# Kernel optimization log

Measured on AMD Instinct MI355X. Metric: run time of the kernel, lower is better.

Reference implementation:

```python
import jax, jax.numpy as jnp
import numpy as np

IN_DIM = 2048
OUT_DIM = 2048
GRID_SIZE = 8
BATCH = 4096
LN_EPS = 1e-5


def setup_inputs() -> dict:
    key = jax.random.key(0)
    k_x, k_w = jax.random.split(key)
    x = jax.random.normal(k_x, (BATCH, IN_DIM), dtype=jnp.float32)
    spline_weight = jax.random.normal(k_w, (OUT_DIM, IN_DIM, GRID_SIZE), dtype=jnp.float32) * 0.1
    return {
        "x": x,
        "ln_weight": jnp.ones((IN_DIM,), jnp.float32),
        "ln_bias": jnp.zeros((IN_DIM,), jnp.float32),
        "spline_weight": spline_weight,
        "scale_base": jnp.ones((OUT_DIM, IN_DIM), jnp.float32),
        "bias": jnp.zeros((OUT_DIM,), jnp.float32),
        "rbf_beta": jnp.full((1,), 2.0, jnp.float32),
        "grid": jnp.linspace(-1.0, 1.0, GRID_SIZE, dtype=jnp.float32),
    }


def reference(x, ln_weight, ln_bias, spline_weight, scale_base, bias, rbf_beta, grid):
    # LayerNorm over last dim (eps=1e-5, elementwise affine)
    mu = jnp.mean(x, axis=-1, keepdims=True)
    var = jnp.mean(jnp.square(x - mu), axis=-1, keepdims=True)
    xn = (x - mu) * jax.lax.rsqrt(var + LN_EPS) * ln_weight + ln_bias  # (B, in)

    beta = jnp.clip(rbf_beta, 0.5, 6.0)  # (1,)
    # RBF basis: (B, in, G)
    basis = jnp.exp(-jnp.square(xn[..., None] - grid) * beta)

    # Torch einsum('bdig,oid->bod') broadcasts the singleton d of basis against
    # spline_weight's last axis and sums g; after .sum(-1) this equals
    # (sum_g basis) @ (sum_d spline_weight).T
    S = basis.sum(-1)              # (B, in)
    Wd = spline_weight.sum(-1)     # (out, in)
    spline_sum = jnp.einsum('bi,oi->bo', S, Wd)

    base_out = jnp.einsum('bi,oi->bo', xn, scale_base)
    return base_out + spline_sum + bias
```

## Files before the change

### kernel.cpp

```cpp
#include <hip/hip_runtime.h>
#include <hip/hip_bf16.h>
#include <stdint.h>

constexpr int IN_DIM   = 2048;
constexpr int OUT_DIM  = 2048;
constexpr int BATCH    = 4096;
constexpr int KDIM     = 2 * IN_DIM;
constexpr float LN_EPS = 1e-5f;

#define TILE 128
#define BK   64
constexpr int NK    = KDIM / BK;
constexpr int STAGE = TILE * BK;

typedef __attribute__((ext_vector_type(8))) short  short8;
typedef __attribute__((ext_vector_type(4))) float  f32x4;

__device__ __forceinline__ unsigned short f2bf(float f) {
  __hip_bfloat16 h = __float2bfloat16(f);
  return *reinterpret_cast<unsigned short*>(&h);
}
__device__ __forceinline__ unsigned pack2bf(float a, float b) {
  return (unsigned)f2bf(a) | ((unsigned)f2bf(b) << 16);
}

constexpr int SW_F4   = OUT_DIM * IN_DIM * 2;
constexpr int SB_F4   = OUT_DIM * IN_DIM / 4;
constexpr int PACK_BLOCKS = (SW_F4 + SB_F4) / 256;

__global__ __launch_bounds__(256) void prep_kernel(
    const float* __restrict__ x, const float* __restrict__ lnw,
    const float* __restrict__ lnb, const float* __restrict__ betap,
    const float* __restrict__ grid, unsigned short* __restrict__ A,
    const float* __restrict__ sw, const float* __restrict__ sb,
    unsigned* __restrict__ Bu)
{
  const int tid = threadIdx.x;
  if (blockIdx.x < BATCH) {
    const int row = blockIdx.x;
    const float4* xr = reinterpret_cast<const float4*>(x + (size_t)row * IN_DIM);
    float4 v0 = xr[tid];
    float4 v1 = xr[tid + 256];
    float s = (v0.x + v0.y) + (v0.z + v0.w) + (v1.x + v1.y) + (v1.z + v1.w);
    float q = v0.x * v0.x + v0.y * v0.y + v0.z * v0.z + v0.w * v0.w
            + v1.x * v1.x + v1.y * v1.y + v1.z * v1.z + v1.w * v1.w;
    #pragma unroll
    for (int off = 32; off > 0; off >>= 1) {
      s += __shfl_down(s, off, 64);
      q += __shfl_down(q, off, 64);
    }
    __shared__ float red[10];
    const int lane = tid & 63, wv = tid >> 6;
    if (lane == 0) { red[wv] = s; red[4 + wv] = q; }
    __syncthreads();
    if (tid == 0) {
      float ts = (red[0] + red[1]) + (red[2] + red[3]);
      float tq = (red[4] + red[5]) + (red[6] + red[7]);
      float mu  = ts * (1.0f / IN_DIM);
      float var = tq * (1.0f / IN_DIM) - mu * mu;
      red[8] = mu;
      red[9] = rsqrtf(var + LN_EPS);
    }
    __syncthreads();
    const float mu = red[8], rs = red[9];
    const float beta = fminf(fmaxf(betap[0], 0.5f), 6.0f);
    float g[8];
    #pragma unroll
    for (int i = 0; i < 8; i++) g[i] = grid[i];
    const float4* w4 = reinterpret_cast<const float4*>(lnw);
    const float4* b4 = reinterpret_cast<const float4*>(lnb);
    unsigned short* Ar = A + (size_t)row * KDIM;
    #pragma unroll
    for (int h = 0; h < 2; h++) {
      const int idx = tid + h * 256;
      float4 xv  = (h == 0) ? v0 : v1;
      float4 wv4 = w4[idx];
      float4 bv4 = b4[idx];
      float xa[4] = {xv.x, xv.y, xv.z, xv.w};
      float wa[4] = {wv4.x, wv4.y, wv4.z, wv4.w};
      float ba[4] = {bv4.x, bv4.y, bv4.z, bv4.w};
      float xn[4], S[4];
      #pragma unroll
      for (int c = 0; c < 4; c++) {
        float xnv = (xa[c] - mu) * rs * wa[c] + ba[c];
        xn[c] = xnv;
        float acc = 0.f;
        #pragma unroll
        for (int gg = 0; gg < 8; gg++) {
          float d = xnv - g[gg];
          acc += __expf(-beta * d * d);
        }
        S[c] = acc;
      }
      uint2 px, ps;
      px.x = pack2bf(xn[0], xn[1]);
      px.y = pack2bf(xn[2], xn[3]);
      ps.x = pack2bf(S[0], S[1]);
      ps.y = pack2bf(S[2], S[3]);
      *reinterpret_cast<uint2*>(Ar + idx * 4) = px;
      *reinterpret_cast<uint2*>(Ar + IN_DIM + idx * 4) = ps;
    }
  } else {
    const int g = (blockIdx.x - BATCH) * 256 + tid;
    const int lane = tid & 63;
    if (g < SW_F4) {
      float4 v = reinterpret_cast<const float4*>(sw)[g];
      float s = (v.x + v.y) + (v.z + v.w);
      s += __shfl_xor(s, 1, 64);
      float hi = __shfl_down(s, 2, 64);
      if ((lane & 3) == 0) {
        const int i_lin = g >> 1;
        const int o = i_lin >> 11;
        const int i = i_lin & (IN_DIM - 1);
        Bu[(size_t)o * (KDIM / 2) + (IN_DIM / 2) + (i >> 1)] = pack2bf(s, hi);
      }
    } else {
      const int t = g - SW_F4;
      float4 v = reinterpret_cast<const float4*>(sb)[t];
      const int o  = t >> 9;
      const int i4 = t & 511;
      uint2 u;
      u.x = pack2bf(v.x, v.y);
      u.y = pack2bf(v.z, v.w);
      *reinterpret_cast<uint2*>(&Bu[(size_t)o * (KDIM / 2) + i4 * 2]) = u;
    }
  }
}

__device__ __forceinline__ void gld_lds16(const unsigned short* g, unsigned short* l) {
  __builtin_amdgcn_global_load_lds(
      (const __attribute__((address_space(1))) void*)g,
      (__attribute__((address_space(3))) void*)l, 16, 0, 0);
}

__global__ __launch_bounds__(256) void gemm_kernel(
    const unsigned short* __restrict__ A, const unsigned short* __restrict__ Bm,
    const float* __restrict__ bias, float* __restrict__ out)
{
  __shared__ __align__(16) unsigned short As[2 * STAGE];
  __shared__ __align__(16) unsigned short Bs[2 * STAGE];
  const int tid  = threadIdx.x;
  const int lane = tid & 63;
  const int wv   = tid >> 6;
  const int wr   = wv >> 1;
  const int wc   = wv & 1;
  const int gid = blockIdx.x;
  const int sq  = gid & 7;
  const int q   = gid >> 3;
  const int m0  = ((sq >> 1) * 8 + (q >> 3)) * TILE;
  const int n0  = ((sq & 1) * 8 + (q & 7)) * TILE;
  const int lrow = lane & 15;
  const int lkq  = lane >> 4;

  f32x4 acc[4][4] = {};

  const unsigned short* Ap[4];
  const unsigned short* Bp[4];
  unsigned short* ldsA[4];
  unsigned short* ldsB[4];
  #pragma unroll
  for (int j = 0; j < 4; j++) {
    const int seg  = j * 256 + wv * 64 + lane;
    const int row  = seg >> 3;
    const int gcol = ((seg & 7) ^ (row & 7)) * 8;
    Ap[j] = A  + (size_t)(m0 + row) * KDIM + gcol;
    Bp[j] = Bm + (size_t)(n0 + row) * KDIM + gcol;
    ldsA[j] = &As[(j * 256 + wv * 64) * 8];
    ldsB[j] = &Bs[(j * 256 + wv * 64) * 8];
  }

  #pragma unroll
  for (int j = 0; j < 4; j++) gld_lds16(Ap[j], ldsA[j]);
  #pragma unroll
  for (int j = 0; j < 4; j++) gld_lds16(Bp[j], ldsB[j]);

  #pragma unroll 1
  for (int kt = 0; kt < NK; kt++) {
    __syncthreads();
    const int cur = (kt & 1) * STAGE;
    if (kt + 1 < NK) {
      const int nxt = ((kt + 1) & 1) * STAGE;
      const int koff = (kt + 1) * BK;
      #pragma unroll
      for (int j = 0; j < 4; j++) gld_lds16(Ap[j] + koff, ldsA[j] + nxt);
      #pragma unroll
      for (int j = 0; j < 4; j++) gld_lds16(Bp[j] + koff, ldsB[j] + nxt);
    }

    short8 af[2][4], bf[2][4];
    #pragma unroll
    for (int h = 0; h < 2; h++) {
      #pragma unroll
      for (int mi = 0; mi < 4; mi++) {
        const int r = wr * 64 + mi * 16 + lrow;
        af[h][mi] = *reinterpret_cast<const short8*>(
            &As[cur + r * BK + (((h << 2) | lkq) ^ (lrow & 7)) * 8]);
      }
      #pragma unroll
      for (int ni = 0; ni < 4; ni++) {
        const int r = wc * 64 + ni * 16 + lrow;
        bf[h][ni] = *reinterpret_cast<const short8*>(
            &Bs[cur + r * BK + (((h << 2) | lkq) ^ (lrow & 7)) * 8]);
      }
    }
    #pragma unroll
    for (int h = 0; h < 2; h++)
      #pragma unroll
      for (int mi = 0; mi < 4; mi++)
        #pragma unroll
        for (int ni = 0; ni < 4; ni++)
          acc[mi][ni] = __builtin_amdgcn_mfma_f32_16x16x32_bf16(
              af[h][mi], bf[h][ni], acc[mi][ni], 0, 0, 0);
  }

  const int rb = (lane >> 4) * 4;
  #pragma unroll
  for (int ni = 0; ni < 4; ni++) {
    const int col = n0 + wc * 64 + ni * 16 + lrow;
    const float bv = bias[col];
    #pragma unroll
    for (int mi = 0; mi < 4; mi++) {
      const int rowm = m0 + wr * 64 + mi * 16 + rb;
      #pragma unroll
      for (int r = 0; r < 4; r++)
        out[(size_t)(rowm + r) * OUT_DIM + col] = acc[mi][ni][r] + bv;
    }
  }
}

extern "C" void kernel_launch(void* const* d_in, const int* in_sizes, int n_in,
                              void* d_out, int out_size, void* d_ws, size_t ws_size,
                              hipStream_t stream) {
  const float* x    = (const float*)d_in[0];
  const float* lnw  = (const float*)d_in[1];
  const float* lnb  = (const float*)d_in[2];
  const float* sw   = (const float*)d_in[3];
  const float* sb   = (const float*)d_in[4];
  const float* bias = (const float*)d_in[5];
  const float* beta = (const float*)d_in[6];
  const float* grid = (const float*)d_in[7];
  float* out = (float*)d_out;

  unsigned short* A = (unsigned short*)d_ws;
  unsigned short* B = A + (size_t)BATCH * KDIM;

  hipLaunchKernelGGL(prep_kernel, dim3(BATCH + PACK_BLOCKS), dim3(256), 0, stream,
                     x, lnw, lnb, beta, grid, A, sw, sb, (unsigned*)B);
  hipLaunchKernelGGL(gemm_kernel, dim3((BATCH / TILE) * (OUT_DIM / TILE)), dim3(256), 0, stream,
                     A, B, bias, out);
}
```

Measured before the change: 304.0 us.

## Use 256x128 tiles with 512 threads and a triple-buffered split-phase pipeline

Grows the GEMM block tile to 256x128 with 8 waves and replaces the double-buffered loop with a three-stage LDS ring. Each K-step is split into two half-phases, with prefetch issued between the fragment reads, explicit waitcnt/barrier scheduling and raised priority around the MFMA bursts. The aim is to hide global-load latency and cut sync overhead per FLOP. In exchange it uses more LDS per block and relies on hand-written waitcnt counts, which could be fragile.

```diff
diff --git a/kernel.cpp b/kernel.cpp
--- a/kernel.cpp
+++ b/kernel.cpp
@@ -8,10 +8,12 @@
 constexpr int KDIM     = 2 * IN_DIM;
 constexpr float LN_EPS = 1e-5f;
 
-#define TILE 128
-#define BK   64
-constexpr int NK    = KDIM / BK;
-constexpr int STAGE = TILE * BK;
+#define BM 256
+#define BN 128
+#define BK 64
+constexpr int NK     = KDIM / BK;
+constexpr int ASTAGE = BM * BK;
+constexpr int BSTAGE = BN * BK;
 
 typedef __attribute__((ext_vector_type(8))) short  short8;
 typedef __attribute__((ext_vector_type(4))) float  f32x4;
@@ -133,84 +135,137 @@
       (__attribute__((address_space(3))) void*)l, 16, 0, 0);
 }
 
-__global__ __launch_bounds__(256) void gemm_kernel(
+__global__ __launch_bounds__(512, 2) void gemm_kernel(
     const unsigned short* __restrict__ A, const unsigned short* __restrict__ Bm,
     const float* __restrict__ bias, float* __restrict__ out)
 {
-  __shared__ __align__(16) unsigned short As[2 * STAGE];
-  __shared__ __align__(16) unsigned short Bs[2 * STAGE];
+  __shared__ __align__(16) unsigned short As[3 * ASTAGE];
+  __shared__ __align__(16) unsigned short Bs[3 * BSTAGE];
   const int tid  = threadIdx.x;
   const int lane = tid & 63;
   const int wv   = tid >> 6;
   const int wr   = wv >> 1;
   const int wc   = wv & 1;
-  const int gid = blockIdx.x;
-  const int sq  = gid & 7;
-  const int q   = gid >> 3;
-  const int m0  = ((sq >> 1) * 8 + (q >> 3)) * TILE;
-  const int n0  = ((sq & 1) * 8 + (q & 7)) * TILE;
   const int lrow = lane & 15;
   const int lkq  = lane >> 4;
 
+  const int gid = blockIdx.x;
+  const int x   = gid & 7;
+  const int q   = gid >> 3;
+  const int m0  = ((x >> 1) * 4 + (q >> 3)) * BM;
+  const int n0  = ((x & 1) * 8 + (q & 7)) * BN;
+
   f32x4 acc[4][4] = {};
 
-  const unsigned short* Ap[4];
-  const unsigned short* Bp[4];
-  unsigned short* ldsA[4];
-  unsigned short* ldsB[4];
+  const unsigned short* Ag[4];
+  const unsigned short* Bg[2];
+  int ldsAo[4], ldsBo[2];
   #pragma unroll
   for (int j = 0; j < 4; j++) {
-    const int seg  = j * 256 + wv * 64 + lane;
-    const int row  = seg >> 3;
-    const int gcol = ((seg & 7) ^ (row & 7)) * 8;
-    Ap[j] = A  + (size_t)(m0 + row) * KDIM + gcol;
-    Bp[j] = Bm + (size_t)(n0 + row) * KDIM + gcol;
-    ldsA[j] = &As[(j * 256 + wv * 64) * 8];
-    ldsB[j] = &Bs[(j * 256 + wv * 64) * 8];
-  }
-
-  #pragma unroll
-  for (int j = 0; j < 4; j++) gld_lds16(Ap[j], ldsA[j]);
-  #pragma unroll
-  for (int j = 0; j < 4; j++) gld_lds16(Bp[j], ldsB[j]);
+    const int row  = j * 64 + (tid >> 3);
+    const int colg = ((tid & 7) ^ (row & 7)) * 8;
+    Ag[j]   = A + (size_t)(m0 + row) * KDIM + colg;
+    ldsAo[j] = (j * 512 + wv * 64) * 8;
+  }
+  #pragma unroll
+  for (int j = 0; j < 2; j++) {
+    const int row  = j * 64 + (tid >> 3);
+    const int colg = ((tid & 7) ^ (row & 7)) * 8;
+    Bg[j]   = Bm + (size_t)(n0 + row) * KDIM + colg;
+    ldsBo[j] = (j * 512 + wv * 64) * 8;
+  }
+
+  #pragma unroll
+  for (int j = 0; j < 4; j++) gld_lds16(Ag[j], &As[ldsAo[j]]);
+  #pragma unroll
+  for (int j = 0; j < 2; j++) gld_lds16(Bg[j], &Bs[ldsBo[j]]);
+  #pragma unroll
+  for (int j = 0; j < 4; j++) gld_lds16(Ag[j] + BK, &As[ASTAGE + ldsAo[j]]);
+  #pragma unroll
+  for (int j = 0; j < 2; j++) gld_lds16(Bg[j] + BK, &Bs[BSTAGE + ldsBo[j]]);
+  asm volatile("s_waitcnt vmcnt(6)" ::: "memory");
+  __builtin_amdgcn_s_barrier();
+
+  int rb_cur = 0;
+  int rb_pf  = 2;
 
   #pragma unroll 1
-  for (int kt = 0; kt < NK; kt++) {
-    __syncthreads();
-    const int cur = (kt & 1) * STAGE;
-    if (kt + 1 < NK) {
-      const int nxt = ((kt + 1) & 1) * STAGE;
-      const int koff = (kt + 1) * BK;
+  for (int t = 0; t < NK; ++t) {
+    const unsigned short* ar = &As[rb_cur * ASTAGE];
+    const unsigned short* br = &Bs[rb_cur * BSTAGE];
+    unsigned short*       aw = &As[rb_pf  * ASTAGE];
+    unsigned short*       bw = &Bs[rb_pf  * BSTAGE];
+    const int  koff = (t + 2) * BK;
+    const bool pf   = (t + 2 < NK);
+
+    short8 af[4], bf[4];
+
+    #pragma unroll
+    for (int mi = 0; mi < 4; mi++) {
+      const int r = wr * 64 + mi * 16 + lrow;
+      af[mi] = *reinterpret_cast<const short8*>(
+          &ar[r * BK + ((lkq ^ (lrow & 7)) * 8)]);
+    }
+    #pragma unroll
+    for (int ni = 0; ni < 4; ni++) {
+      const int r = wc * 64 + ni * 16 + lrow;
+      bf[ni] = *reinterpret_cast<const short8*>(
+          &br[r * BK + ((lkq ^ (lrow & 7)) * 8)]);
+    }
+    if (pf) {
+      gld_lds16(Ag[0] + koff, &aw[ldsAo[0]]);
+      gld_lds16(Ag[1] + koff, &aw[ldsAo[1]]);
+      gld_lds16(Bg[0] + koff, &bw[ldsBo[0]]);
+    }
+    __builtin_amdgcn_s_barrier();
+    asm volatile("s_waitcnt lgkmcnt(0)" ::: "memory");
+    __builtin_amdgcn_s_setprio(1);
+    #pragma unroll
+    for (int mi = 0; mi < 4; mi++)
       #pragma unroll
-      for (int j = 0; j < 4; j++) gld_lds16(Ap[j] + koff, ldsA[j] + nxt);
+      for (int ni = 0; ni < 4; ni++)
+        acc[mi][ni] = __builtin_amdgcn_mfma_f32_16x16x32_bf16(
+            af[mi], bf[ni], acc[mi][ni], 0, 0, 0);
+    __builtin_amdgcn_s_setprio(0);
+    __builtin_amdgcn_s_barrier();
+
+    #pragma unroll
+    for (int mi = 0; mi < 4; mi++) {
+      const int r = wr * 64 + mi * 16 + lrow;
+      af[mi] = *reinterpret_cast<const short8*>(
+          &ar[r * BK + (((4 | lkq) ^ (lrow & 7)) * 8)]);
+    }
+    #pragma unroll
+    for (int ni = 0; ni < 4; ni++) {
+      const int r = wc * 64 + ni * 16 + lrow;
+      bf[ni] = *reinterpret_cast<const short8*>(
+          &br[r * BK + (((4 | lkq) ^ (lrow & 7)) * 8)]);
+    }
+    if (pf) {
+      gld_lds16(Ag[2] + koff, &aw[ldsAo[2]]);
+      gld_lds16(Ag[3] + koff, &aw[ldsAo[3]]);
+      gld_lds16(Bg[1] + koff, &bw[ldsBo[1]]);
+    }
+    __builtin_amdgcn_s_barrier();
+    asm volatile("s_waitcnt lgkmcnt(0)" ::: "memory");
+    __builtin_amdgcn_s_setprio(1);
+    #pragma unroll
+    for (int mi = 0; mi < 4; mi++)
       #pragma unroll
-      for (int j = 0; j < 4; j++) gld_lds16(Bp[j] + koff, ldsB[j] + nxt);
-    }
-
-    short8 af[2][4], bf[2][4];
-    #pragma unroll
-    for (int h = 0; h < 2; h++) {
-      #pragma unroll
-      for (int mi = 0; mi < 4; mi++) {
-        const int r = wr * 64 + mi * 16 + lrow;
-        af[h][mi] = *reinterpret_cast<const short8*>(
-            &As[cur + r * BK + (((h << 2) | lkq) ^ (lrow & 7)) * 8]);
-      }
-      #pragma unroll
-      for (int ni = 0; ni < 4; ni++) {
-        const int r = wc * 64 + ni * 16 + lrow;
-        bf[h][ni] = *reinterpret_cast<const short8*>(
-            &Bs[cur + r * BK + (((h << 2) | lkq) ^ (lrow & 7)) * 8]);
-      }
-    }
-    #pragma unroll
-    for (int h = 0; h < 2; h++)
-      #pragma unroll
-      for (int mi = 0; mi < 4; mi++)
-        #pragma unroll
-        for (int ni = 0; ni < 4; ni++)
-          acc[mi][ni] = __builtin_amdgcn_mfma_f32_16x16x32_bf16(
-              af[h][mi], bf[h][ni], acc[mi][ni], 0, 0, 0);
+      for (int ni = 0; ni < 4; ni++)
+        acc[mi][ni] = __builtin_amdgcn_mfma_f32_16x16x32_bf16(
+            af[mi], bf[ni], acc[mi][ni], 0, 0, 0);
+    __builtin_amdgcn_s_setprio(0);
+
+    if (pf) {
+      asm volatile("s_waitcnt vmcnt(6)" ::: "memory");
+    } else if (t + 2 == NK) {
+      asm volatile("s_waitcnt vmcnt(0)" ::: "memory");
+    }
+    __builtin_amdgcn_s_barrier();
+
+    rb_cur = (rb_cur == 2) ? 0 : rb_cur + 1;
+    rb_pf  = (rb_pf  == 2) ? 0 : rb_pf  + 1;
   }
 
   const int rb = (lane >> 4) * 4;
@@ -246,6 +301,6 @@
 
   hipLaunchKernelGGL(prep_kernel, dim3(BATCH + PACK_BLOCKS), dim3(256), 0, stream,
                      x, lnw, lnb, beta, grid, A, sw, sb, (unsigned*)B);
-  hipLaunchKernelGGL(gemm_kernel, dim3((BATCH / TILE) * (OUT_DIM / TILE)), dim3(256), 0, stream,
+  hipLaunchKernelGGL(gemm_kernel, dim3((BATCH / BM) * (OUT_DIM / BN)), dim3(512), 0, stream,
                      A, B, bias, out);
 }
```

Result: no change. 310.0 us (+2.0%).

## Use 256x256 tiles with split-K, 4-stage LDS pipeline and atomic accumulation

Applied to the files above, without the earlier changes.

Replaces the 128x128, 256-thread GEMM tile with a 256x256 tile run by 512 threads, splitting K in two so the grid keeps 256 blocks. It adds a 4-slot global-to-LDS prefetch pipeline with explicit waitcnt, barriers and setprio around the MFMA block. The output is zeroed in the prep kernel and both K halves accumulate into it with float atomicAdd. This raises data reuse per LDS load and hides memory latency better, at the cost of the zeroing pass, atomic write traffic and nondeterministic summation order.

```diff
diff --git a/kernel.cpp b/kernel.cpp
--- a/kernel.cpp
+++ b/kernel.cpp
@@ -8,10 +8,13 @@
 constexpr int KDIM     = 2 * IN_DIM;
 constexpr float LN_EPS = 1e-5f;
 
-#define TILE 128
-#define BK   64
-constexpr int NK    = KDIM / BK;
-constexpr int STAGE = TILE * BK;
+#define BM 256
+#define BN 256
+#define BKH 32
+constexpr int KSPLIT = 2;
+constexpr int K_PER  = KDIM / KSPLIT;
+constexpr int NKH    = K_PER / BKH;
+constexpr int SLOT   = BM * BKH;
 
 typedef __attribute__((ext_vector_type(8))) short  short8;
 typedef __attribute__((ext_vector_type(4))) float  f32x4;
@@ -24,16 +27,23 @@
   return (unsigned)f2bf(a) | ((unsigned)f2bf(b) << 16);
 }
 
+__device__ __forceinline__ void gld_lds16(const unsigned short* g, unsigned short* l) {
+  __builtin_amdgcn_global_load_lds(
+      (const __attribute__((address_space(1))) void*)g,
+      (__attribute__((address_space(3))) void*)l, 16, 0, 0);
+}
+
 constexpr int SW_F4   = OUT_DIM * IN_DIM * 2;
 constexpr int SB_F4   = OUT_DIM * IN_DIM / 4;
 constexpr int PACK_BLOCKS = (SW_F4 + SB_F4) / 256;
+constexpr int ZERO_BLOCKS = (BATCH * OUT_DIM) / (256 * 16);
 
 __global__ __launch_bounds__(256) void prep_kernel(
     const float* __restrict__ x, const float* __restrict__ lnw,
     const float* __restrict__ lnb, const float* __restrict__ betap,
     const float* __restrict__ grid, unsigned short* __restrict__ A,
     const float* __restrict__ sw, const float* __restrict__ sb,
-    unsigned* __restrict__ Bu)
+    unsigned* __restrict__ Bu, float* __restrict__ outz)
 {
   const int tid = threadIdx.x;
   if (blockIdx.x < BATCH) {
@@ -100,7 +110,7 @@
       *reinterpret_cast<uint2*>(Ar + idx * 4) = px;
       *reinterpret_cast<uint2*>(Ar + IN_DIM + idx * 4) = ps;
     }
-  } else {
+  } else if (blockIdx.x < BATCH + PACK_BLOCKS) {
     const int g = (blockIdx.x - BATCH) * 256 + tid;
     const int lane = tid & 63;
     if (g < SW_F4) {
@@ -124,106 +134,114 @@
       u.y = pack2bf(v.z, v.w);
       *reinterpret_cast<uint2*>(&Bu[(size_t)o * (KDIM / 2) + i4 * 2]) = u;
     }
-  }
-}
-
-__device__ __forceinline__ void gld_lds16(const unsigned short* g, unsigned short* l) {
-  __builtin_amdgcn_global_load_lds(
-      (const __attribute__((address_space(1))) void*)g,
-      (__attribute__((address_space(3))) void*)l, 16, 0, 0);
-}
-
-__global__ __launch_bounds__(256) void gemm_kernel(
+  } else {
+    const int zb = blockIdx.x - BATCH - PACK_BLOCKS;
+    float4 z = {0.f, 0.f, 0.f, 0.f};
+    float4* o4 = reinterpret_cast<float4*>(outz) + ((size_t)zb * 256 + tid) * 4;
+    o4[0] = z; o4[1] = z; o4[2] = z; o4[3] = z;
+  }
+}
+
+__global__ __launch_bounds__(512, 2) void gemm_kernel(
     const unsigned short* __restrict__ A, const unsigned short* __restrict__ Bm,
     const float* __restrict__ bias, float* __restrict__ out)
 {
-  __shared__ __align__(16) unsigned short As[2 * STAGE];
-  __shared__ __align__(16) unsigned short Bs[2 * STAGE];
+  __shared__ __align__(16) unsigned short As[4 * SLOT];
+  __shared__ __align__(16) unsigned short Bs[4 * SLOT];
   const int tid  = threadIdx.x;
   const int lane = tid & 63;
   const int wv   = tid >> 6;
-  const int wr   = wv >> 1;
-  const int wc   = wv & 1;
-  const int gid = blockIdx.x;
-  const int sq  = gid & 7;
-  const int q   = gid >> 3;
-  const int m0  = ((sq >> 1) * 8 + (q >> 3)) * TILE;
-  const int n0  = ((sq & 1) * 8 + (q & 7)) * TILE;
+  const int wr   = wv >> 2;
+  const int wc   = wv & 3;
   const int lrow = lane & 15;
   const int lkq  = lane >> 4;
 
-  f32x4 acc[4][4] = {};
-
-  const unsigned short* Ap[4];
-  const unsigned short* Bp[4];
-  unsigned short* ldsA[4];
-  unsigned short* ldsB[4];
+  const int gid = blockIdx.x;
+  const int xcd = gid & 7;
+  const int j   = gid >> 3;
+  const int kk  = xcd >> 2;
+  const int m0  = (((xcd & 3) << 2) + (j >> 3)) * BM;
+  const int n0  = (j & 7) * BN;
+  const int kbase = kk * K_PER;
+
+  f32x4 acc[8][4] = {};
+
+  const unsigned short* Ag[2];
+  const unsigned short* Bg[2];
+  int ldsO[2];
   #pragma unroll
-  for (int j = 0; j < 4; j++) {
-    const int seg  = j * 256 + wv * 64 + lane;
-    const int row  = seg >> 3;
-    const int gcol = ((seg & 7) ^ (row & 7)) * 8;
-    Ap[j] = A  + (size_t)(m0 + row) * KDIM + gcol;
-    Bp[j] = Bm + (size_t)(n0 + row) * KDIM + gcol;
-    ldsA[j] = &As[(j * 256 + wv * 64) * 8];
-    ldsB[j] = &Bs[(j * 256 + wv * 64) * 8];
+  for (int t = 0; t < 2; t++) {
+    const int r = (wv * 2 + t) * 16 + (lane >> 2);
+    const int g = (lane & 3) ^ ((lane >> 2) & 3);
+    Ag[t]   = A  + (size_t)(m0 + r) * KDIM + kbase + g * 8;
+    Bg[t]   = Bm + (size_t)(n0 + r) * KDIM + kbase + g * 8;
+    ldsO[t] = (wv * 2 + t) * 512;
   }
 
   #pragma unroll
-  for (int j = 0; j < 4; j++) gld_lds16(Ap[j], ldsA[j]);
-  #pragma unroll
-  for (int j = 0; j < 4; j++) gld_lds16(Bp[j], ldsB[j]);
+  for (int p = 0; p < 3; p++) {
+    const int d = p * SLOT, kc = p * BKH;
+    gld_lds16(Ag[0] + kc, &As[d + ldsO[0]]);
+    gld_lds16(Ag[1] + kc, &As[d + ldsO[1]]);
+    gld_lds16(Bg[0] + kc, &Bs[d + ldsO[0]]);
+    gld_lds16(Bg[1] + kc, &Bs[d + ldsO[1]]);
+  }
+  asm volatile("s_waitcnt vmcnt(8)" ::: "memory");
+  __builtin_amdgcn_s_barrier();
+  asm volatile("" ::: "memory");
+
+  const int swz  = (lkq ^ (lrow & 3)) << 3;
+  const int aoff = (wr * 128 + lrow) * 32 + swz;
+  const int boff = (wc * 64  + lrow) * 32 + swz;
 
   #pragma unroll 1
-  for (int kt = 0; kt < NK; kt++) {
-    __syncthreads();
-    const int cur = (kt & 1) * STAGE;
-    if (kt + 1 < NK) {
-      const int nxt = ((kt + 1) & 1) * STAGE;
-      const int koff = (kt + 1) * BK;
+  for (int kh = 0; kh < NKH; kh++) {
+    const int slot = (kh & 3) * SLOT;
+    short8 af[8], bf[4];
+    #pragma unroll
+    for (int mi = 0; mi < 8; mi++)
+      af[mi] = *reinterpret_cast<const short8*>(&As[slot + aoff + mi * 512]);
+    #pragma unroll
+    for (int ni = 0; ni < 4; ni++)
+      bf[ni] = *reinterpret_cast<const short8*>(&Bs[slot + boff + ni * 512]);
+
+    if (kh + 3 < NKH) {
+      const int d = ((kh + 3) & 3) * SLOT, kc = (kh + 3) * BKH;
+      gld_lds16(Ag[0] + kc, &As[d + ldsO[0]]);
+      gld_lds16(Ag[1] + kc, &As[d + ldsO[1]]);
+      gld_lds16(Bg[0] + kc, &Bs[d + ldsO[0]]);
+      gld_lds16(Bg[1] + kc, &Bs[d + ldsO[1]]);
+    }
+
+    asm volatile("s_waitcnt lgkmcnt(0)" ::: "memory");
+    __builtin_amdgcn_sched_barrier(0);
+    __builtin_amdgcn_s_setprio(1);
+    #pragma unroll
+    for (int mi = 0; mi < 8; mi++)
       #pragma unroll
-      for (int j = 0; j < 4; j++) gld_lds16(Ap[j] + koff, ldsA[j] + nxt);
-      #pragma unroll
-      for (int j = 0; j < 4; j++) gld_lds16(Bp[j] + koff, ldsB[j] + nxt);
-    }
-
-    short8 af[2][4], bf[2][4];
-    #pragma unroll
-    for (int h = 0; h < 2; h++) {
-      #pragma unroll
-      for (int mi = 0; mi < 4; mi++) {
-        const int r = wr * 64 + mi * 16 + lrow;
-        af[h][mi] = *reinterpret_cast<const short8*>(
-            &As[cur + r * BK + (((h << 2) | lkq) ^ (lrow & 7)) * 8]);
-      }
-      #pragma unroll
-      for (int ni = 0; ni < 4; ni++) {
-        const int r = wc * 64 + ni * 16 + lrow;
-        bf[h][ni] = *reinterpret_cast<const short8*>(
-            &Bs[cur + r * BK + (((h << 2) | lkq) ^ (lrow & 7)) * 8]);
-      }
-    }
-    #pragma unroll
-    for (int h = 0; h < 2; h++)
-      #pragma unroll
-      for (int mi = 0; mi < 4; mi++)
-        #pragma unroll
-        for (int ni = 0; ni < 4; ni++)
-          acc[mi][ni] = __builtin_amdgcn_mfma_f32_16x16x32_bf16(
-              af[h][mi], bf[h][ni], acc[mi][ni], 0, 0, 0);
+      for (int ni = 0; ni < 4; ni++)
+        acc[mi][ni] = __builtin_amdgcn_mfma_f32_16x16x32_bf16(
+            af[mi], bf[ni], acc[mi][ni], 0, 0, 0);
+    __builtin_amdgcn_s_setprio(0);
+
+    if (kh < NKH - 3)       asm volatile("s_waitcnt vmcnt(8)" ::: "memory");
+    else if (kh == NKH - 3) asm volatile("s_waitcnt vmcnt(4)" ::: "memory");
+    else if (kh == NKH - 2) asm volatile("s_waitcnt vmcnt(0)" ::: "memory");
+    __builtin_amdgcn_s_barrier();
+    asm volatile("" ::: "memory");
   }
 
   const int rb = (lane >> 4) * 4;
   #pragma unroll
   for (int ni = 0; ni < 4; ni++) {
     const int col = n0 + wc * 64 + ni * 16 + lrow;
-    const float bv = bias[col];
-    #pragma unroll
-    for (int mi = 0; mi < 4; mi++) {
-      const int rowm = m0 + wr * 64 + mi * 16 + rb;
+    const float bv = (kk == 0) ? bias[col] : 0.0f;
+    #pragma unroll
+    for (int mi = 0; mi < 8; mi++) {
+      const int rowm = m0 + wr * 128 + mi * 16 + rb;
       #pragma unroll
       for (int r = 0; r < 4; r++)
-        out[(size_t)(rowm + r) * OUT_DIM + col] = acc[mi][ni][r] + bv;
+        atomicAdd(&out[(size_t)(rowm + r) * OUT_DIM + col], acc[mi][ni][r] + bv);
     }
   }
 }
@@ -244,8 +262,9 @@
   unsigned short* A = (unsigned short*)d_ws;
   unsigned short* B = A + (size_t)BATCH * KDIM;
 
-  hipLaunchKernelGGL(prep_kernel, dim3(BATCH + PACK_BLOCKS), dim3(256), 0, stream,
-                     x, lnw, lnb, beta, grid, A, sw, sb, (unsigned*)B);
-  hipLaunchKernelGGL(gemm_kernel, dim3((BATCH / TILE) * (OUT_DIM / TILE)), dim3(256), 0, stream,
+  hipLaunchKernelGGL(prep_kernel, dim3(BATCH + PACK_BLOCKS + ZERO_BLOCKS), dim3(256), 0,
+                     stream, x, lnw, lnb, beta, grid, A, sw, sb, (unsigned*)B, out);
+  hipLaunchKernelGGL(gemm_kernel,
+                     dim3((BATCH / BM) * (OUT_DIM / BN) * KSPLIT), dim3(512), 0, stream,
                      A, B, bias, out);
 }
```

New measurement: 347.1 us. 14.2% more time.
